# Kernel optimization log

Hardware: AMD Instinct MI355X
Metric: run time of the kernel (lower is better)

The kernel has to match this reference:

```python
import jax, jax.numpy as jnp
import numpy as np


def setup_inputs() -> dict:
    key = jax.random.key(0)
    k_x, k_w, k_W, k_b, k_idx = jax.random.split(key, 5)
    B, C, N, K, O = 2, 32, 40962, 25, 64
    x = jax.random.normal(k_x, (B, C, N), dtype=jnp.float32)
    neigh_weights = jax.random.uniform(k_w, (N, K, 3), dtype=jnp.float32)
    W = jax.random.normal(k_W, (O, K * C), dtype=jnp.float32) * 0.02
    b = jax.random.normal(k_b, (O,), dtype=jnp.float32) * 0.02
    neigh_indices = jax.random.randint(k_idx, (N, K, 3), 0, N, dtype=jnp.int32)
    return {"x": x, "neigh_weights": neigh_weights, "W": W, "b": b,
            "neigh_indices": neigh_indices}


def reference(x, neigh_weights, W, b, neigh_indices):
    # x: (B, C, N); neigh_indices/neigh_weights: (N, K, 3); W: (O, C*K); b: (O,)
    B, C, N = x.shape
    _, K, _ = neigh_indices.shape
    # Gather neighbor features: (B, C, N, K, 3)
    mat = x[:, :, neigh_indices]
    # Barycentric weighted sum over the 3 triangle vertices -> (B, C, N, K)
    s = jnp.einsum('bcnkt,nkt->bcnk', mat, neigh_weights)
    # Permute to (B, N, C, K) and apply Linear(C*K -> O)
    feat = s.transpose(0, 2, 1, 3).reshape(B * N, C * K)
    out = feat @ W.T + b  # (B*N, O)
    out = out.reshape(B, N, -1).transpose(0, 2, 1)  # (B, O, N)
    return out
```

## Files before the change

kernel.cpp:

```cpp
#include <hip/hip_runtime.h>
#include <hip/hip_fp16.h>

typedef __attribute__((ext_vector_type(8))) _Float16 half8;
typedef __attribute__((ext_vector_type(4))) float f32x4;

union U2H2 { unsigned int u; __half2 h; };

static __device__ __forceinline__ unsigned int pack2h(float a, float b) {
    U2H2 c; c.h = __floats2half2_rn(a, b); return c.u;
}
static __device__ __forceinline__ __half2 u_as_h2(unsigned int u) {
    U2H2 c; c.u = u; return c.h;
}
static __device__ __forceinline__ __half2 hi16(unsigned int u) {
    return u_as_h2(__builtin_amdgcn_perm(u, u, 0x03020302u));
}

#define SWZ(row, slot) \
    ((slot) ^ ((row) & 3) ^ (((row) >> 2) & 3) ^ (((row) >> 5) & 1))

#define LDS_BARRIER()                                                \
    do {                                                             \
        asm volatile("s_waitcnt lgkmcnt(0)" ::: "memory");           \
        __builtin_amdgcn_s_barrier();                                \
        __builtin_amdgcn_sched_barrier(0);                           \
    } while (0)

__global__ __launch_bounds__(256) void prep_all(const float* __restrict__ x,
                                                const float* __restrict__ W,
                                                unsigned short* __restrict__ xth,
                                                unsigned short* __restrict__ Wrh,
                                                int N, int nT) {
    int bid = blockIdx.x, tid = threadIdx.x;
    if (bid >= nT) {
        int k = bid - nT;
#pragma unroll
        for (int it = 0; it < 8; ++it) {
            int r = tid + 256 * it;
            int o = r >> 5, c = r & 31;
            __half h = __float2half(W[o * 800 + c * 25 + k]);
            Wrh[k * 2048 + r] = *reinterpret_cast<unsigned short*>(&h);
        }
        return;
    }
    __shared__ float t[2][32][65];
    int n0 = bid * 64;
#pragma unroll
    for (int i = 0; i < 16; ++i) {
        int e = tid + 256 * i;
        int b = e >> 11, c = (e >> 6) & 31, nl = e & 63;
        int n = n0 + nl;
        t[b][c][nl] = (n < N) ? x[(size_t)(b * 32 + c) * N + n] : 0.f;
    }
    __syncthreads();
    int nl = tid >> 2, q = tid & 3, n = n0 + nl;
    if (n < N) {
#pragma unroll
        for (int b = 0; b < 2; ++b) {
            uint4 p;
            p.x = pack2h(t[b][q * 8 + 0][nl], t[b][q * 8 + 1][nl]);
            p.y = pack2h(t[b][q * 8 + 2][nl], t[b][q * 8 + 3][nl]);
            p.z = pack2h(t[b][q * 8 + 4][nl], t[b][q * 8 + 5][nl]);
            p.w = pack2h(t[b][q * 8 + 6][nl], t[b][q * 8 + 7][nl]);
            *reinterpret_cast<uint4*>(xth + ((size_t)n * 64 + b * 32 + q * 8)) = p;
        }
    }
}

__global__ __launch_bounds__(256) void fused_main(
    const unsigned short* __restrict__ xth,
    const unsigned short* __restrict__ Wrh,
    const float* __restrict__ bias,
    const int* __restrict__ nidx,
    const float* __restrict__ nw,
    float* __restrict__ out,
    int N)
{
    __shared__ unsigned int idxw[32 * 75];
    __shared__ __align__(16) unsigned char sA[2][4096];
    __shared__ __align__(16) unsigned char sB[2][4096];

    const int tid = threadIdx.x;
    const int n0 = blockIdx.x * 32;

#pragma unroll
    for (int it = 0; it < 10; ++it) {
        int e = tid + 256 * it;
        if (e < 2400) {
            int n = n0 + e / 75;
            unsigned int u = 0;
            if (n < N) {
                size_t s = (size_t)n0 * 75 + e;
                int j = nidx[s];
                __half hw = __float2half(nw[s]);
                u = (unsigned int)j |
                    ((unsigned int)*reinterpret_cast<unsigned short*>(&hw) << 16);
            }
            idxw[e] = u;
        }
    }
    __syncthreads();

    const int nl = tid >> 3;
    const int p  = tid & 7;
    const int grow = (p >> 2) * 32 + nl;
    const int q = p & 3;
    const int wr_off = grow * 64 + (SWZ(grow, q) << 4);

    const int sbo = (tid >> 2) * 64 + (SWZ((tid >> 2), (tid & 3)) << 4);

    const int l = tid & 63, wv = tid >> 6, c16 = l & 15, g = l >> 4;
    const int arow = 16 * wv + c16;
    const int rd_a = arow * 64 + (SWZ(arow, g) << 4);

    const unsigned short* xg = xth + p * 8;
    const unsigned int* iprow = &idxw[nl * 75];

    unsigned int ru[3][3];
    uint4 rg[3][3];
    uint4 rB;

    f32x4 acc[4];
#pragma unroll
    for (int ot = 0; ot < 4; ++ot) acc[ot] = (f32x4){0.f, 0.f, 0.f, 0.f};

    rB = *reinterpret_cast<const uint4*>(Wrh + tid * 8);
#pragma unroll
    for (int kk = 0; kk < 3; ++kk)
#pragma unroll
        for (int t = 0; t < 3; ++t) ru[kk][t] = iprow[kk * 3 + t];
#pragma unroll
    for (int kk = 0; kk < 3; ++kk)
#pragma unroll
        for (int t = 0; t < 3; ++t)
            rg[kk][t] = *reinterpret_cast<const uint4*>(xg + (ru[kk][t] & 0xffffu) * 64);

#pragma unroll
    for (int k = 0; k < 25; ++k) {
        const int gb = k % 3, buf = k & 1;

        *reinterpret_cast<uint4*>(&sB[buf][sbo]) = rB;
        if (k + 1 < 25)
            rB = *reinterpret_cast<const uint4*>(Wrh + (k + 1) * 2048 + tid * 8);

        {
            __half2 w0 = hi16(ru[gb][0]), w1 = hi16(ru[gb][1]), w2 = hi16(ru[gb][2]);
            uint4 v0 = rg[gb][0], v1 = rg[gb][1], v2 = rg[gb][2];
            uint4 pk; U2H2 c;
            c.h = __hfma2(u_as_h2(v0.x), w0, __hfma2(u_as_h2(v1.x), w1, __hmul2(u_as_h2(v2.x), w2)));
            pk.x = c.u;
            c.h = __hfma2(u_as_h2(v0.y), w0, __hfma2(u_as_h2(v1.y), w1, __hmul2(u_as_h2(v2.y), w2)));
            pk.y = c.u;
            c.h = __hfma2(u_as_h2(v0.z), w0, __hfma2(u_as_h2(v1.z), w1, __hmul2(u_as_h2(v2.z), w2)));
            pk.z = c.u;
            c.h = __hfma2(u_as_h2(v0.w), w0, __hfma2(u_as_h2(v1.w), w1, __hmul2(u_as_h2(v2.w), w2)));
            pk.w = c.u;
            *reinterpret_cast<uint4*>(&sA[buf][wr_off]) = pk;
        }

        if (k + 3 < 25) {
#pragma unroll
            for (int t = 0; t < 3; ++t) ru[gb][t] = iprow[(k + 3) * 3 + t];
        }

        LDS_BARRIER();

        if (k + 3 < 25) {
#pragma unroll
            for (int t = 0; t < 3; ++t)
                rg[gb][t] = *reinterpret_cast<const uint4*>(xg + (ru[gb][t] & 0xffffu) * 64);
        }

        {
            half8 af = *reinterpret_cast<const half8*>(&sA[buf][rd_a]);
            __builtin_amdgcn_s_setprio(1);
#pragma unroll
            for (int ot = 0; ot < 4; ++ot) {
                int orow = ot * 16 + c16;
                half8 bf = *reinterpret_cast<const half8*>(
                    &sB[buf][orow * 64 + (SWZ(orow, g) << 4)]);
                acc[ot] = __builtin_amdgcn_mfma_f32_16x16x32_f16(af, bf, acc[ot], 0, 0, 0);
            }
            __builtin_amdgcn_s_setprio(0);
        }
    }

#pragma unroll
    for (int ot = 0; ot < 4; ++ot) {
        int o = ot * 16 + c16;
        float bv = bias[o];
#pragma unroll
        for (int i = 0; i < 4; ++i) {
            int mrow = 16 * wv + 4 * g + i;
            int b = mrow >> 5, nn = n0 + (mrow & 31);
            if (nn < N) out[((size_t)b * 64 + o) * N + nn] = acc[ot][i] + bv;
        }
    }
}

extern "C" void kernel_launch(void* const* d_in, const int* in_sizes, int n_in,
                              void* d_out, int out_size, void* d_ws, size_t ws_size,
                              hipStream_t stream) {
    const float* x    = (const float*)d_in[0];
    const float* nw   = (const float*)d_in[1];
    const float* W    = (const float*)d_in[2];
    const float* bias = (const float*)d_in[3];
    const int*   nidx = (const int*)d_in[4];
    float* out = (float*)d_out;

    int N = in_sizes[0] / 64;

    unsigned short* xth = (unsigned short*)d_ws;
    unsigned short* Wrh = xth + (size_t)N * 64;

    int nT = (N + 63) / 64;
    prep_all<<<nT + 25, 256, 0, stream>>>(x, W, xth, Wrh, N, nT);

    fused_main<<<(N + 31) / 32, 256, 0, stream>>>(xth, Wrh, bias, nidx, nw, out, N);
}
```

Before: 58.03 us.

## Process two K-slices per barrier period with padded index layout and zero-padded weights

The main loop now handles two neighbour slices per synchronization period, so there are 13 barriers instead of 25 and eight MFMAs per barrier instead of four. To make this work, the weights are zero-padded to 26 slices and the index/weight table is re-laid out with 4-word rows per k, which allows vectorized 16-byte LDS reads. The LDS tiles double in size and use a new XOR swizzle. The cost is more LDS and more registers for the in-flight gathers (12 uint4 per thread), which may reduce occupancy, plus one extra padded slice of work that is mostly zeros.

```diff
diff --git a/kernel.cpp b/kernel.cpp
--- a/kernel.cpp
+++ b/kernel.cpp
@@ -15,9 +15,6 @@
 static __device__ __forceinline__ __half2 hi16(unsigned int u) {
     return u_as_h2(__builtin_amdgcn_perm(u, u, 0x03020302u));
 }
-
-#define SWZ(row, slot) \
-    ((slot) ^ ((row) & 3) ^ (((row) >> 2) & 3) ^ (((row) >> 5) & 1))
 
 #define LDS_BARRIER()                                                \
     do {                                                             \
@@ -38,7 +35,8 @@
         for (int it = 0; it < 8; ++it) {
             int r = tid + 256 * it;
             int o = r >> 5, c = r & 31;
-            __half h = __float2half(W[o * 800 + c * 25 + k]);
+            float v = (k < 25) ? W[o * 800 + c * 25 + k] : 0.f;
+            __half h = __float2half(v);
             Wrh[k * 2048 + r] = *reinterpret_cast<unsigned short*>(&h);
         }
         return;
@@ -76,18 +74,26 @@
     float* __restrict__ out,
     int N)
 {
-    __shared__ unsigned int idxw[32 * 75];
-    __shared__ __align__(16) unsigned char sA[2][4096];
-    __shared__ __align__(16) unsigned char sB[2][4096];
+    __shared__ unsigned int idxw[32 * 26 * 4];
+    __shared__ __align__(16) unsigned char sA[2][8192];
+    __shared__ __align__(16) unsigned char sB[2][8192];
 
     const int tid = threadIdx.x;
     const int n0 = blockIdx.x * 32;
 
+#pragma unroll
+    for (int it = 0; it < 13; ++it) {
+        int e = tid + 256 * it;
+        if (e < 3328) idxw[e] = 0u;
+    }
+    __syncthreads();
 #pragma unroll
     for (int it = 0; it < 10; ++it) {
         int e = tid + 256 * it;
         if (e < 2400) {
-            int n = n0 + e / 75;
+            int nl = e / 75, r = e - nl * 75;
+            int kk = r / 3, t = r - kk * 3;
+            int n = n0 + nl;
             unsigned int u = 0;
             if (n < N) {
                 size_t s = (size_t)n0 * 75 + e;
@@ -96,94 +102,151 @@
                 u = (unsigned int)j |
                     ((unsigned int)*reinterpret_cast<unsigned short*>(&hw) << 16);
             }
-            idxw[e] = u;
+            idxw[nl * 104 + kk * 4 + t] = u;
         }
     }
     __syncthreads();
 
     const int nl = tid >> 3;
-    const int p  = tid & 7;
-    const int grow = (p >> 2) * 32 + nl;
-    const int q = p & 3;
-    const int wr_off = grow * 64 + (SWZ(grow, q) << 4);
-
-    const int sbo = (tid >> 2) * 64 + (SWZ((tid >> 2), (tid & 3)) << 4);
+    const int p8 = tid & 7;
+    const int grow = (p8 >> 2) * 32 + nl;
+    const int gq = p8 & 3;
+    const int wr_k0 = grow * 128 + ((((gq << 1) | 0) ^ (grow & 7)) << 4);
+    const int wr_k1 = wr_k0 ^ 16;
+
+    const int borow = tid >> 2, bq = tid & 3;
+    const int sbo_k0 = borow * 128 + ((((bq << 1) | 0) ^ (borow & 7)) << 4);
+    const int sbo_k1 = sbo_k0 ^ 16;
+    const int gbo = borow * 32 + bq * 8;
 
     const int l = tid & 63, wv = tid >> 6, c16 = l & 15, g = l >> 4;
     const int arow = 16 * wv + c16;
-    const int rd_a = arow * 64 + (SWZ(arow, g) << 4);
-
-    const unsigned short* xg = xth + p * 8;
-    const unsigned int* iprow = &idxw[nl * 75];
-
-    unsigned int ru[3][3];
-    uint4 rg[3][3];
-    uint4 rB;
+    const int rd_a0 = arow * 128 + ((((g << 1) | 0) ^ (arow & 7)) << 4);
+    const int rd_a1 = rd_a0 ^ 16;
+    const int bf_b0 = c16 * 128 + ((((g << 1) | 0) ^ (c16 & 7)) << 4);
+    const int bf_b1 = bf_b0 ^ 16;
+
+    const unsigned short* xg = xth + p8 * 8;
+    const unsigned int* iprow = &idxw[nl * 104];
+
+    unsigned int ruA[6], ruB[6];
+    uint4 rgA[6], rgB[6];
+    uint4 rBv0, rBv1;
 
     f32x4 acc[4];
 #pragma unroll
     for (int ot = 0; ot < 4; ++ot) acc[ot] = (f32x4){0.f, 0.f, 0.f, 0.f};
 
-    rB = *reinterpret_cast<const uint4*>(Wrh + tid * 8);
-#pragma unroll
-    for (int kk = 0; kk < 3; ++kk)
-#pragma unroll
-        for (int t = 0; t < 3; ++t) ru[kk][t] = iprow[kk * 3 + t];
-#pragma unroll
-    for (int kk = 0; kk < 3; ++kk)
-#pragma unroll
-        for (int t = 0; t < 3; ++t)
-            rg[kk][t] = *reinterpret_cast<const uint4*>(xg + (ru[kk][t] & 0xffffu) * 64);
-
-#pragma unroll
-    for (int k = 0; k < 25; ++k) {
-        const int gb = k % 3, buf = k & 1;
-
-        *reinterpret_cast<uint4*>(&sB[buf][sbo]) = rB;
-        if (k + 1 < 25)
-            rB = *reinterpret_cast<const uint4*>(Wrh + (k + 1) * 2048 + tid * 8);
-
-        {
-            __half2 w0 = hi16(ru[gb][0]), w1 = hi16(ru[gb][1]), w2 = hi16(ru[gb][2]);
-            uint4 v0 = rg[gb][0], v1 = rg[gb][1], v2 = rg[gb][2];
-            uint4 pk; U2H2 c;
-            c.h = __hfma2(u_as_h2(v0.x), w0, __hfma2(u_as_h2(v1.x), w1, __hmul2(u_as_h2(v2.x), w2)));
-            pk.x = c.u;
-            c.h = __hfma2(u_as_h2(v0.y), w0, __hfma2(u_as_h2(v1.y), w1, __hmul2(u_as_h2(v2.y), w2)));
-            pk.y = c.u;
-            c.h = __hfma2(u_as_h2(v0.z), w0, __hfma2(u_as_h2(v1.z), w1, __hmul2(u_as_h2(v2.z), w2)));
-            pk.z = c.u;
-            c.h = __hfma2(u_as_h2(v0.w), w0, __hfma2(u_as_h2(v1.w), w1, __hmul2(u_as_h2(v2.w), w2)));
-            pk.w = c.u;
-            *reinterpret_cast<uint4*>(&sA[buf][wr_off]) = pk;
-        }
-
-        if (k + 3 < 25) {
-#pragma unroll
-            for (int t = 0; t < 3; ++t) ru[gb][t] = iprow[(k + 3) * 3 + t];
-        }
-
-        LDS_BARRIER();
-
-        if (k + 3 < 25) {
-#pragma unroll
-            for (int t = 0; t < 3; ++t)
-                rg[gb][t] = *reinterpret_cast<const uint4*>(xg + (ru[gb][t] & 0xffffu) * 64);
-        }
-
-        {
-            half8 af = *reinterpret_cast<const half8*>(&sA[buf][rd_a]);
-            __builtin_amdgcn_s_setprio(1);
-#pragma unroll
-            for (int ot = 0; ot < 4; ++ot) {
-                int orow = ot * 16 + c16;
-                half8 bf = *reinterpret_cast<const half8*>(
-                    &sB[buf][orow * 64 + (SWZ(orow, g) << 4)]);
-                acc[ot] = __builtin_amdgcn_mfma_f32_16x16x32_f16(af, bf, acc[ot], 0, 0, 0);
-            }
-            __builtin_amdgcn_s_setprio(0);
-        }
-    }
+    rBv0 = *reinterpret_cast<const uint4*>(Wrh + gbo);
+    rBv1 = *reinterpret_cast<const uint4*>(Wrh + 2048 + gbo);
+    {
+        uint4 i0 = *reinterpret_cast<const uint4*>(iprow + 0);
+        uint4 i1 = *reinterpret_cast<const uint4*>(iprow + 4);
+        uint4 i2 = *reinterpret_cast<const uint4*>(iprow + 8);
+        uint4 i3 = *reinterpret_cast<const uint4*>(iprow + 12);
+        ruA[0] = i0.x; ruA[1] = i0.y; ruA[2] = i0.z;
+        ruA[3] = i1.x; ruA[4] = i1.y; ruA[5] = i1.z;
+        ruB[0] = i2.x; ruB[1] = i2.y; ruB[2] = i2.z;
+        ruB[3] = i3.x; ruB[4] = i3.y; ruB[5] = i3.z;
+    }
+#pragma unroll
+    for (int t = 0; t < 6; ++t)
+        rgA[t] = *reinterpret_cast<const uint4*>(xg + (ruA[t] & 0xffffu) * 64);
+#pragma unroll
+    for (int t = 0; t < 6; ++t)
+        rgB[t] = *reinterpret_cast<const uint4*>(xg + (ruB[t] & 0xffffu) * 64);
+
+#define HFMA_STORE(U0, U1, U2, V0, V1, V2, OFF)                                    \
+    do {                                                                           \
+        __half2 w0 = hi16(U0), w1 = hi16(U1), w2 = hi16(U2);                       \
+        uint4 pk; U2H2 c;                                                          \
+        c.h = __hfma2(u_as_h2((V0).x), w0,                                         \
+              __hfma2(u_as_h2((V1).x), w1, __hmul2(u_as_h2((V2).x), w2)));         \
+        pk.x = c.u;                                                                \
+        c.h = __hfma2(u_as_h2((V0).y), w0,                                         \
+              __hfma2(u_as_h2((V1).y), w1, __hmul2(u_as_h2((V2).y), w2)));         \
+        pk.y = c.u;                                                                \
+        c.h = __hfma2(u_as_h2((V0).z), w0,                                         \
+              __hfma2(u_as_h2((V1).z), w1, __hmul2(u_as_h2((V2).z), w2)));         \
+        pk.z = c.u;                                                                \
+        c.h = __hfma2(u_as_h2((V0).w), w0,                                         \
+              __hfma2(u_as_h2((V1).w), w1, __hmul2(u_as_h2((V2).w), w2)));         \
+        pk.w = c.u;                                                                \
+        *reinterpret_cast<uint4*>(OFF) = pk;                                       \
+    } while (0)
+
+#define PERIOD(P, RG, RU)                                                          \
+    do {                                                                           \
+        const int pb = (P) & 1;                                                    \
+                                        \
+        *reinterpret_cast<uint4*>(&sB[pb][sbo_k0]) = rBv0;                         \
+        *reinterpret_cast<uint4*>(&sB[pb][sbo_k1]) = rBv1;                         \
+        {                                                                          \
+            int kb0 = 2 * (P) + 2; kb0 = kb0 > 25 ? 25 : kb0;                      \
+            int kb1 = 2 * (P) + 3; kb1 = kb1 > 25 ? 25 : kb1;                      \
+            rBv0 = *reinterpret_cast<const uint4*>(Wrh + kb0 * 2048 + gbo);        \
+            rBv1 = *reinterpret_cast<const uint4*>(Wrh + kb1 * 2048 + gbo);        \
+        }                                                                          \
+                                       \
+        HFMA_STORE(RU[0], RU[1], RU[2], RG[0], RG[1], RG[2], &sA[pb][wr_k0]);      \
+        HFMA_STORE(RU[3], RU[4], RU[5], RG[3], RG[4], RG[5], &sA[pb][wr_k1]);      \
+                         \
+        uint4 niq0, niq1;                                                          \
+        {                                                                          \
+            int ka = 2 * (P) + 4; ka = ka > 25 ? 25 : ka;                          \
+            int kb = 2 * (P) + 5; kb = kb > 25 ? 25 : kb;                          \
+            niq0 = *reinterpret_cast<const uint4*>(iprow + ka * 4);                \
+            niq1 = *reinterpret_cast<const uint4*>(iprow + kb * 4);                \
+        }                                                                          \
+        LDS_BARRIER();                                                             \
+           \
+        RU[0] = niq0.x; RU[1] = niq0.y; RU[2] = niq0.z;                            \
+        RU[3] = niq1.x; RU[4] = niq1.y; RU[5] = niq1.z;                            \
+        RG[0] = *reinterpret_cast<const uint4*>(xg + (RU[0] & 0xffffu) * 64);      \
+        RG[1] = *reinterpret_cast<const uint4*>(xg + (RU[1] & 0xffffu) * 64);      \
+        RG[2] = *reinterpret_cast<const uint4*>(xg + (RU[2] & 0xffffu) * 64);      \
+        RG[3] = *reinterpret_cast<const uint4*>(xg + (RU[3] & 0xffffu) * 64);      \
+        RG[4] = *reinterpret_cast<const uint4*>(xg + (RU[4] & 0xffffu) * 64);      \
+        RG[5] = *reinterpret_cast<const uint4*>(xg + (RU[5] & 0xffffu) * 64);      \
+                                                   \
+        {                                                                          \
+            half8 af0 = *reinterpret_cast<const half8*>(&sA[pb][rd_a0]);           \
+            half8 af1 = *reinterpret_cast<const half8*>(&sA[pb][rd_a1]);           \
+            __builtin_amdgcn_s_setprio(1);                                         \
+            _Pragma("unroll")                                                      \
+            for (int ot = 0; ot < 4; ++ot) {                                       \
+                half8 bf0 = *reinterpret_cast<const half8*>(                       \
+                    &sB[pb][bf_b0 + ot * 2048]);                                   \
+                acc[ot] = __builtin_amdgcn_mfma_f32_16x16x32_f16(af0, bf0,         \
+                                                                 acc[ot], 0, 0, 0);\
+            }                                                                      \
+            _Pragma("unroll")                                                      \
+            for (int ot = 0; ot < 4; ++ot) {                                       \
+                half8 bf1 = *reinterpret_cast<const half8*>(                       \
+                    &sB[pb][bf_b1 + ot * 2048]);                                   \
+                acc[ot] = __builtin_amdgcn_mfma_f32_16x16x32_f16(af1, bf1,         \
+                                                                 acc[ot], 0, 0, 0);\
+            }                                                                      \
+            __builtin_amdgcn_s_setprio(0);                                         \
+        }                                                                          \
+    } while (0)
+
+    PERIOD(0, rgA, ruA);
+    PERIOD(1, rgB, ruB);
+    PERIOD(2, rgA, ruA);
+    PERIOD(3, rgB, ruB);
+    PERIOD(4, rgA, ruA);
+    PERIOD(5, rgB, ruB);
+    PERIOD(6, rgA, ruA);
+    PERIOD(7, rgB, ruB);
+    PERIOD(8, rgA, ruA);
+    PERIOD(9, rgB, ruB);
+    PERIOD(10, rgA, ruA);
+    PERIOD(11, rgB, ruB);
+    PERIOD(12, rgA, ruA);
+
+#undef PERIOD
+#undef HFMA_STORE
 
 #pragma unroll
     for (int ot = 0; ot < 4; ++ot) {
@@ -214,7 +277,7 @@
     unsigned short* Wrh = xth + (size_t)N * 64;
 
     int nT = (N + 63) / 64;
-    prep_all<<<nT + 25, 256, 0, stream>>>(x, W, xth, Wrh, N, nT);
+    prep_all<<<nT + 26, 256, 0, stream>>>(x, W, xth, Wrh, N, nT);
 
     fused_main<<<(N + 31) / 32, 256, 0, stream>>>(xth, Wrh, bias, nidx, nw, out, N);
 }
```

Measured after the change: 59.35 us. +2.3%, slower.

## Halve fused block to 16 vertices and 128 threads with padded index layout

Applied to the files above, without the earlier changes.

Shrinks each fused block from 32 to 16 vertices with 128 threads (2 waves, one per batch), doubling the grid, so each thread now stages two W fragments per k step. The index/weight table is padded to 4-word groups so each k's three entries load as one vector LDS read. Next-stage gathers are issued after the MFMAs instead of before them, and the s_setprio calls and one swizzle term are removed. More blocks should improve latency hiding and occupancy. In exchange, each block reloads the full W tile per k for half as many output rows, and zeroing the table adds an extra barrier.

```diff
diff --git a/kernel.cpp b/kernel.cpp
--- a/kernel.cpp
+++ b/kernel.cpp
@@ -16,8 +16,7 @@
     return u_as_h2(__builtin_amdgcn_perm(u, u, 0x03020302u));
 }
 
-#define SWZ(row, slot) \
-    ((slot) ^ ((row) & 3) ^ (((row) >> 2) & 3) ^ (((row) >> 5) & 1))
+#define SWZ(row, slot) ((slot) ^ ((row) & 3) ^ (((row) >> 2) & 3))
 
 #define LDS_BARRIER()                                                \
     do {                                                             \
@@ -67,7 +66,7 @@
     }
 }
 
-__global__ __launch_bounds__(256) void fused_main(
+__global__ __launch_bounds__(128) void fused_main(
     const unsigned short* __restrict__ xth,
     const unsigned short* __restrict__ Wrh,
     const float* __restrict__ bias,
@@ -76,18 +75,26 @@
     float* __restrict__ out,
     int N)
 {
-    __shared__ unsigned int idxw[32 * 75];
-    __shared__ __align__(16) unsigned char sA[2][4096];
+    __shared__ unsigned int idxw[16 * 104];
+    __shared__ __align__(16) unsigned char sA[2][2048];
     __shared__ __align__(16) unsigned char sB[2][4096];
 
     const int tid = threadIdx.x;
-    const int n0 = blockIdx.x * 32;
-
+    const int n0 = blockIdx.x * 16;
+
+#pragma unroll
+    for (int it = 0; it < 13; ++it) {
+        int e = tid + 128 * it;
+        if (e < 1664) idxw[e] = 0u;
+    }
+    __syncthreads();
 #pragma unroll
     for (int it = 0; it < 10; ++it) {
-        int e = tid + 256 * it;
-        if (e < 2400) {
-            int n = n0 + e / 75;
+        int e = tid + 128 * it;
+        if (e < 1200) {
+            int nl = e / 75, r = e - nl * 75;
+            int kk = r / 3, t = r - kk * 3;
+            int n = n0 + nl;
             unsigned int u = 0;
             if (n < N) {
                 size_t s = (size_t)n0 * 75 + e;
@@ -96,39 +103,45 @@
                 u = (unsigned int)j |
                     ((unsigned int)*reinterpret_cast<unsigned short*>(&hw) << 16);
             }
-            idxw[e] = u;
+            idxw[nl * 104 + kk * 4 + t] = u;
         }
     }
     __syncthreads();
 
     const int nl = tid >> 3;
-    const int p  = tid & 7;
-    const int grow = (p >> 2) * 32 + nl;
-    const int q = p & 3;
-    const int wr_off = grow * 64 + (SWZ(grow, q) << 4);
-
-    const int sbo = (tid >> 2) * 64 + (SWZ((tid >> 2), (tid & 3)) << 4);
+    const int p8 = tid & 7;
+    const int grow = (p8 >> 2) * 16 + nl;
+    const int gq = p8 & 3;
+    const int wr_off = grow * 64 + (SWZ(grow, gq) << 4);
+
+    const int s1 = tid + 128;
+    const int sbo0 = (tid >> 2) * 64 + (SWZ((tid >> 2), (tid & 3)) << 4);
+    const int sbo1 = (s1 >> 2) * 64 + (SWZ((s1 >> 2), (s1 & 3)) << 4);
+    const int gbo0 = (tid >> 2) * 32 + (tid & 3) * 8;
+    const int gbo1 = (s1 >> 2) * 32 + (s1 & 3) * 8;
 
     const int l = tid & 63, wv = tid >> 6, c16 = l & 15, g = l >> 4;
     const int arow = 16 * wv + c16;
     const int rd_a = arow * 64 + (SWZ(arow, g) << 4);
 
-    const unsigned short* xg = xth + p * 8;
-    const unsigned int* iprow = &idxw[nl * 75];
+    const unsigned short* xg = xth + p8 * 8;
+    const unsigned int* iprow = &idxw[nl * 104];
 
     unsigned int ru[3][3];
     uint4 rg[3][3];
-    uint4 rB;
+    uint4 rB0, rB1;
 
     f32x4 acc[4];
 #pragma unroll
     for (int ot = 0; ot < 4; ++ot) acc[ot] = (f32x4){0.f, 0.f, 0.f, 0.f};
 
-    rB = *reinterpret_cast<const uint4*>(Wrh + tid * 8);
-#pragma unroll
-    for (int kk = 0; kk < 3; ++kk)
-#pragma unroll
-        for (int t = 0; t < 3; ++t) ru[kk][t] = iprow[kk * 3 + t];
+    rB0 = *reinterpret_cast<const uint4*>(Wrh + gbo0);
+    rB1 = *reinterpret_cast<const uint4*>(Wrh + gbo1);
+#pragma unroll
+    for (int kk = 0; kk < 3; ++kk) {
+        uint4 iq = *reinterpret_cast<const uint4*>(iprow + kk * 4);
+        ru[kk][0] = iq.x; ru[kk][1] = iq.y; ru[kk][2] = iq.z;
+    }
 #pragma unroll
     for (int kk = 0; kk < 3; ++kk)
 #pragma unroll
@@ -139,9 +152,12 @@
     for (int k = 0; k < 25; ++k) {
         const int gb = k % 3, buf = k & 1;
 
-        *reinterpret_cast<uint4*>(&sB[buf][sbo]) = rB;
-        if (k + 1 < 25)
-            rB = *reinterpret_cast<const uint4*>(Wrh + (k + 1) * 2048 + tid * 8);
+        *reinterpret_cast<uint4*>(&sB[buf][sbo0]) = rB0;
+        *reinterpret_cast<uint4*>(&sB[buf][sbo1]) = rB1;
+        if (k + 1 < 25) {
+            rB0 = *reinterpret_cast<const uint4*>(Wrh + (k + 1) * 2048 + gbo0);
+            rB1 = *reinterpret_cast<const uint4*>(Wrh + (k + 1) * 2048 + gbo1);
+        }
 
         {
             __half2 w0 = hi16(ru[gb][0]), w1 = hi16(ru[gb][1]), w2 = hi16(ru[gb][2]);
@@ -158,22 +174,16 @@
             *reinterpret_cast<uint4*>(&sA[buf][wr_off]) = pk;
         }
 
-        if (k + 3 < 25) {
-#pragma unroll
-            for (int t = 0; t < 3; ++t) ru[gb][t] = iprow[(k + 3) * 3 + t];
-        }
-
         LDS_BARRIER();
 
-        if (k + 3 < 25) {
-#pragma unroll
-            for (int t = 0; t < 3; ++t)
-                rg[gb][t] = *reinterpret_cast<const uint4*>(xg + (ru[gb][t] & 0xffffu) * 64);
+        uint4 niq;
+        {
+            int ka = (k + 3 < 25) ? k + 3 : 24;
+            niq = *reinterpret_cast<const uint4*>(iprow + ka * 4);
         }
 
         {
             half8 af = *reinterpret_cast<const half8*>(&sA[buf][rd_a]);
-            __builtin_amdgcn_s_setprio(1);
 #pragma unroll
             for (int ot = 0; ot < 4; ++ot) {
                 int orow = ot * 16 + c16;
@@ -181,7 +191,13 @@
                     &sB[buf][orow * 64 + (SWZ(orow, g) << 4)]);
                 acc[ot] = __builtin_amdgcn_mfma_f32_16x16x32_f16(af, bf, acc[ot], 0, 0, 0);
             }
-            __builtin_amdgcn_s_setprio(0);
+        }
+
+        if (k + 3 < 25) {
+            ru[gb][0] = niq.x; ru[gb][1] = niq.y; ru[gb][2] = niq.z;
+#pragma unroll
+            for (int t = 0; t < 3; ++t)
+                rg[gb][t] = *reinterpret_cast<const uint4*>(xg + (ru[gb][t] & 0xffffu) * 64);
         }
     }
 
@@ -191,9 +207,8 @@
         float bv = bias[o];
 #pragma unroll
         for (int i = 0; i < 4; ++i) {
-            int mrow = 16 * wv + 4 * g + i;
-            int b = mrow >> 5, nn = n0 + (mrow & 31);
-            if (nn < N) out[((size_t)b * 64 + o) * N + nn] = acc[ot][i] + bv;
+            int n = n0 + 4 * g + i;
+            if (n < N) out[((size_t)wv * 64 + o) * N + n] = acc[ot][i] + bv;
         }
     }
 }
@@ -216,5 +231,5 @@
     int nT = (N + 63) / 64;
     prep_all<<<nT + 25, 256, 0, stream>>>(x, W, xth, Wrh, N, nT);
 
-    fused_main<<<(N + 31) / 32, 256, 0, stream>>>(xth, Wrh, bias, nidx, nw, out, N);
-}
+    fused_main<<<(N + 15) / 16, 128, 0, stream>>>(xth, Wrh, bias, nidx, nw, out, N);
+}
```

New measurement: 64.01 us. +10.3%, slower.

## Make each wave self-contained: per-wave LDS tiles, registers for W, no block barriers

Applied to the files above, without the earlier changes.

Wrh is re-laid out in prep so each lane can load its MFMA B-fragment straight from global memory into registers. This removes the shared sB buffer. Each wave now builds and reads its own 16-row A tile in LDS, which needs only a wave-local lgkmcnt wait in place of a block-wide barrier. Neighbor indices and weights are read directly from global memory with a short register prefetch, dropping the shared idxw staging and its sync, and the launch bounds request higher occupancy. The trade-offs are redundant W loads per wave, more register pressure, and gathers that are prefetched less deeply (distance 2 instead of 3).

```diff
diff --git a/kernel.cpp b/kernel.cpp
--- a/kernel.cpp
+++ b/kernel.cpp
@@ -12,19 +12,8 @@
 static __device__ __forceinline__ __half2 u_as_h2(unsigned int u) {
     U2H2 c; c.u = u; return c.h;
 }
-static __device__ __forceinline__ __half2 hi16(unsigned int u) {
-    return u_as_h2(__builtin_amdgcn_perm(u, u, 0x03020302u));
-}
-
-#define SWZ(row, slot) \
-    ((slot) ^ ((row) & 3) ^ (((row) >> 2) & 3) ^ (((row) >> 5) & 1))
-
-#define LDS_BARRIER()                                                \
-    do {                                                             \
-        asm volatile("s_waitcnt lgkmcnt(0)" ::: "memory");           \
-        __builtin_amdgcn_s_barrier();                                \
-        __builtin_amdgcn_sched_barrier(0);                           \
-    } while (0)
+
+#define SWZ(row, slot) ((slot) ^ ((row) & 3) ^ (((row) >> 2) & 3))
 
 __global__ __launch_bounds__(256) void prep_all(const float* __restrict__ x,
                                                 const float* __restrict__ W,
@@ -37,7 +26,9 @@
 #pragma unroll
         for (int it = 0; it < 8; ++it) {
             int r = tid + 256 * it;
-            int o = r >> 5, c = r & 31;
+            int ot = r >> 9, lx = (r >> 3) & 63, e = r & 7;
+            int o = ot * 16 + (lx & 15);
+            int c = (lx >> 4) * 8 + e;
             __half h = __float2half(W[o * 800 + c * 25 + k]);
             Wrh[k * 2048 + r] = *reinterpret_cast<unsigned short*>(&h);
         }
@@ -67,7 +58,7 @@
     }
 }
 
-__global__ __launch_bounds__(256) void fused_main(
+__global__ __launch_bounds__(256, 5) void fused_main(
     const unsigned short* __restrict__ xth,
     const unsigned short* __restrict__ Wrh,
     const float* __restrict__ bias,
@@ -76,75 +67,68 @@
     float* __restrict__ out,
     int N)
 {
-    __shared__ unsigned int idxw[32 * 75];
-    __shared__ __align__(16) unsigned char sA[2][4096];
-    __shared__ __align__(16) unsigned char sB[2][4096];
+    __shared__ __align__(16) unsigned char sA[4 * 1024];
 
     const int tid = threadIdx.x;
     const int n0 = blockIdx.x * 32;
 
-#pragma unroll
-    for (int it = 0; it < 10; ++it) {
-        int e = tid + 256 * it;
-        if (e < 2400) {
-            int n = n0 + e / 75;
-            unsigned int u = 0;
-            if (n < N) {
-                size_t s = (size_t)n0 * 75 + e;
-                int j = nidx[s];
-                __half hw = __float2half(nw[s]);
-                u = (unsigned int)j |
-                    ((unsigned int)*reinterpret_cast<unsigned short*>(&hw) << 16);
-            }
-            idxw[e] = u;
-        }
-    }
-    __syncthreads();
-
-    const int nl = tid >> 3;
-    const int p  = tid & 7;
-    const int grow = (p >> 2) * 32 + nl;
-    const int q = p & 3;
-    const int wr_off = grow * 64 + (SWZ(grow, q) << 4);
-
-    const int sbo = (tid >> 2) * 64 + (SWZ((tid >> 2), (tid & 3)) << 4);
-
-    const int l = tid & 63, wv = tid >> 6, c16 = l & 15, g = l >> 4;
-    const int arow = 16 * wv + c16;
-    const int rd_a = arow * 64 + (SWZ(arow, g) << 4);
-
-    const unsigned short* xg = xth + p * 8;
-    const unsigned int* iprow = &idxw[nl * 75];
-
-    unsigned int ru[3][3];
-    uint4 rg[3][3];
-    uint4 rB;
+    const int wv = tid >> 6, l = tid & 63;
+    const int row = tid >> 2;
+    const int q   = tid & 3;
+    const int b0 = row >> 5, nl0 = row & 31;
+    const int c16 = l & 15, g = l >> 4;
+
+    int n = n0 + nl0;
+    int nc = (n < N) ? n : (N - 1);
+    const int*   ib = nidx + (size_t)nc * 75;
+    const float* wb = nw   + (size_t)nc * 75;
+    const unsigned short* xg = xth + b0 * 32 + q * 8;
+
+    unsigned char* sAw = sA + wv * 1024;
+    const int wr_off = (row & 15) * 64 + (SWZ(row, q) << 4);
+    const int rd_a   = c16 * 64 + (SWZ(c16, g) << 4);
+
+    int3   ri[2];
+    float3 rw[2];
+    unsigned int rwh[2][3];
+    uint4  rg[2][3];
+    uint4  rB[4];
 
     f32x4 acc[4];
 #pragma unroll
     for (int ot = 0; ot < 4; ++ot) acc[ot] = (f32x4){0.f, 0.f, 0.f, 0.f};
 
-    rB = *reinterpret_cast<const uint4*>(Wrh + tid * 8);
-#pragma unroll
-    for (int kk = 0; kk < 3; ++kk)
-#pragma unroll
-        for (int t = 0; t < 3; ++t) ru[kk][t] = iprow[kk * 3 + t];
-#pragma unroll
-    for (int kk = 0; kk < 3; ++kk)
-#pragma unroll
-        for (int t = 0; t < 3; ++t)
-            rg[kk][t] = *reinterpret_cast<const uint4*>(xg + (ru[kk][t] & 0xffffu) * 64);
+    {
+        int3 i0 = *reinterpret_cast<const int3*>(ib + 0);
+        float3 w0 = *reinterpret_cast<const float3*>(wb + 0);
+        int3 i1 = *reinterpret_cast<const int3*>(ib + 3);
+        float3 w1 = *reinterpret_cast<const float3*>(wb + 3);
+        rg[0][0] = *reinterpret_cast<const uint4*>(xg + i0.x * 64);
+        rg[0][1] = *reinterpret_cast<const uint4*>(xg + i0.y * 64);
+        rg[0][2] = *reinterpret_cast<const uint4*>(xg + i0.z * 64);
+        rg[1][0] = *reinterpret_cast<const uint4*>(xg + i1.x * 64);
+        rg[1][1] = *reinterpret_cast<const uint4*>(xg + i1.y * 64);
+        rg[1][2] = *reinterpret_cast<const uint4*>(xg + i1.z * 64);
+        rwh[0][0] = pack2h(w0.x, w0.x); rwh[0][1] = pack2h(w0.y, w0.y);
+        rwh[0][2] = pack2h(w0.z, w0.z);
+        rwh[1][0] = pack2h(w1.x, w1.x); rwh[1][1] = pack2h(w1.y, w1.y);
+        rwh[1][2] = pack2h(w1.z, w1.z);
+        ri[0] = *reinterpret_cast<const int3*>(ib + 6);
+        rw[0] = *reinterpret_cast<const float3*>(wb + 6);
+        ri[1] = *reinterpret_cast<const int3*>(ib + 9);
+        rw[1] = *reinterpret_cast<const float3*>(wb + 9);
+#pragma unroll
+        for (int ot = 0; ot < 4; ++ot)
+            rB[ot] = *reinterpret_cast<const uint4*>(Wrh + ot * 512 + l * 8);
+    }
 
 #pragma unroll
     for (int k = 0; k < 25; ++k) {
-        const int gb = k % 3, buf = k & 1;
-
-        *reinterpret_cast<uint4*>(&sB[buf][sbo]) = rB;
-        if (k + 1 < 25)
-            rB = *reinterpret_cast<const uint4*>(Wrh + (k + 1) * 2048 + tid * 8);
+        const int gb = k & 1;
 
         {
-            __half2 w0 = hi16(ru[gb][0]), w1 = hi16(ru[gb][1]), w2 = hi16(ru[gb][2]);
+            __half2 w0 = u_as_h2(rwh[gb][0]), w1 = u_as_h2(rwh[gb][1]),
+                    w2 = u_as_h2(rwh[gb][2]);
             uint4 v0 = rg[gb][0], v1 = rg[gb][1], v2 = rg[gb][2];
             uint4 pk; U2H2 c;
             c.h = __hfma2(u_as_h2(v0.x), w0, __hfma2(u_as_h2(v1.x), w1, __hmul2(u_as_h2(v2.x), w2)));
@@ -155,33 +139,40 @@
             pk.z = c.u;
             c.h = __hfma2(u_as_h2(v0.w), w0, __hfma2(u_as_h2(v1.w), w1, __hmul2(u_as_h2(v2.w), w2)));
             pk.w = c.u;
-            *reinterpret_cast<uint4*>(&sA[buf][wr_off]) = pk;
-        }
-
-        if (k + 3 < 25) {
-#pragma unroll
-            for (int t = 0; t < 3; ++t) ru[gb][t] = iprow[(k + 3) * 3 + t];
-        }
-
-        LDS_BARRIER();
-
-        if (k + 3 < 25) {
-#pragma unroll
-            for (int t = 0; t < 3; ++t)
-                rg[gb][t] = *reinterpret_cast<const uint4*>(xg + (ru[gb][t] & 0xffffu) * 64);
-        }
+            *reinterpret_cast<uint4*>(sAw + wr_off) = pk;
+        }
+
+        if (k + 2 < 25) {
+            rg[gb][0] = *reinterpret_cast<const uint4*>(xg + ri[gb].x * 64);
+            rg[gb][1] = *reinterpret_cast<const uint4*>(xg + ri[gb].y * 64);
+            rg[gb][2] = *reinterpret_cast<const uint4*>(xg + ri[gb].z * 64);
+            rwh[gb][0] = pack2h(rw[gb].x, rw[gb].x);
+            rwh[gb][1] = pack2h(rw[gb].y, rw[gb].y);
+            rwh[gb][2] = pack2h(rw[gb].z, rw[gb].z);
+            int ka = (k + 4 <= 24) ? k + 4 : 24;
+            ri[gb] = *reinterpret_cast<const int3*>(ib + ka * 3);
+            rw[gb] = *reinterpret_cast<const float3*>(wb + ka * 3);
+        }
+
+        asm volatile("s_waitcnt lgkmcnt(0)" ::: "memory");
+        __builtin_amdgcn_sched_barrier(0);
 
         {
-            half8 af = *reinterpret_cast<const half8*>(&sA[buf][rd_a]);
+            half8 af = *reinterpret_cast<const half8*>(sAw + rd_a);
             __builtin_amdgcn_s_setprio(1);
 #pragma unroll
             for (int ot = 0; ot < 4; ++ot) {
-                int orow = ot * 16 + c16;
-                half8 bf = *reinterpret_cast<const half8*>(
-                    &sB[buf][orow * 64 + (SWZ(orow, g) << 4)]);
+                half8 bf = __builtin_bit_cast(half8, rB[ot]);
                 acc[ot] = __builtin_amdgcn_mfma_f32_16x16x32_f16(af, bf, acc[ot], 0, 0, 0);
             }
             __builtin_amdgcn_s_setprio(0);
+        }
+
+        if (k + 1 < 25) {
+#pragma unroll
+            for (int ot = 0; ot < 4; ++ot)
+                rB[ot] = *reinterpret_cast<const uint4*>(
+                    Wrh + (k + 1) * 2048 + ot * 512 + l * 8);
         }
     }
 
```

After: 90.64 us. 1.56x slower.
